# Kernel tuning notes

Measured on AMD Instinct MI355X. Metric: run time of the kernel, lower is better.

The kernel has to match this reference:

```python
import jax, jax.numpy as jnp
import numpy as np

B = 2          # point clouds per batch
N_PER = 80000  # occupied voxels per cloud
D = 64         # voxel grid resolution
K = 27         # 3x3x3 kernel volume
EPS = 1e-5


def _build_maps():
    rng = np.random.RandomState(0)
    coords = []
    for b in range(B):
        flat = rng.choice(D ** 3, N_PER, replace=False)
        x = flat // (D * D); y = (flat // D) % D; z = flat % D
        coords.append(np.stack([np.full(N_PER, b, np.int64), x, y, z], 1))
    coords = np.concatenate(coords, 0)  # [N,4] (batch, x, y, z)

    def make_grid(c, Dd):
        g = np.full(B * Dd ** 3, -1, np.int64)
        key = ((c[:, 0] * Dd + c[:, 1]) * Dd + c[:, 2]) * Dd + c[:, 3]
        g[key] = np.arange(len(c))
        return g

    offsets = np.array([[dx, dy, dz] for dx in (-1, 0, 1) for dy in (-1, 0, 1) for dz in (-1, 0, 1)], np.int64)

    def kernel_map(c, g, Dd):
        # per kernel offset: (input_row, output_row) pairs, padded to M with sentinel n
        n = len(c)
        ins, outs = [], []
        for off in offsets:
            sc = c[:, 1:] + off
            valid = np.all((sc >= 0) & (sc < Dd), 1)
            key = ((c[:, 0] * Dd + sc[:, 0]) * Dd + sc[:, 1]) * Dd + sc[:, 2]
            row = np.where(valid, g[np.clip(key, 0, len(g) - 1)], -1)
            m = row >= 0
            ins.append(row[m]); outs.append(np.nonzero(m)[0])
        M = max(len(a) for a in ins)
        ki = np.full((K, M), n, np.int32); ko = np.full((K, M), n, np.int32)
        for k in range(K):
            ki[k, :len(ins[k])] = ins[k]; ko[k, :len(outs[k])] = outs[k]
        return ki, ko

    km_in, km_out = kernel_map(coords, make_grid(coords, D), D)

    # maxpool k2/s2: each voxel maps to exactly one pooled coordinate floor(c/2)
    Dp = D // 2
    pc = coords.copy(); pc[:, 1:] //= 2
    pkey = ((pc[:, 0] * Dp + pc[:, 1]) * Dp + pc[:, 2]) * Dp + pc[:, 3]
    ukey, pool_seg = np.unique(pkey, return_inverse=True)
    pz = ukey % Dp; py = (ukey // Dp) % Dp; px = (ukey // (Dp * Dp)) % Dp; pb = ukey // (Dp ** 3)
    pcoords = np.stack([pb, px, py, pz], 1)
    km2_in, km2_out = kernel_map(pcoords, make_grid(pcoords, Dp), Dp)
    return len(coords), len(pcoords), km_in, km_out, pool_seg.astype(np.int32), km2_in, km2_out


N, N_POOL, _KM_IN, _KM_OUT, _POOL_SEG, _KM2_IN, _KM2_OUT = _build_maps()


def setup_inputs() -> dict:
    key = jax.random.key(0)
    ks = jax.random.split(key, 4)
    f32 = jnp.float32
    return {
        "feats": jax.random.normal(ks[0], (N, 1), f32),
        "W1": jax.random.normal(ks[1], (K, 1, 64), f32) * 0.2,
        "b1": jnp.zeros((64,), f32),
        "g1": jnp.ones((64,), f32), "be1": jnp.zeros((64,), f32),
        "W2": jax.random.normal(ks[2], (K, 64, 64), f32) * 0.05,
        "b2": jnp.zeros((64,), f32),
        "g2": jnp.ones((64,), f32), "be2": jnp.zeros((64,), f32),
        "W3": jax.random.normal(ks[3], (K, 64, 128), f32) * 0.05,
        "b3": jnp.zeros((128,), f32),
        "g3": jnp.ones((128,), f32), "be3": jnp.zeros((128,), f32),
        "km_in": jnp.asarray(_KM_IN), "km_out": jnp.asarray(_KM_OUT),
        "pool_seg": jnp.asarray(_POOL_SEG),
        "km2_in": jnp.asarray(_KM2_IN), "km2_out": jnp.asarray(_KM2_OUT),
    }


def _sparse_conv(x, ki, ko, W, b):
    # gather-GEMM-scatter per kernel offset; sentinel index n hits padded zero row / dummy out row
    n = x.shape[0]
    xp = jnp.concatenate([x, jnp.zeros((1, x.shape[1]), x.dtype)], 0)
    out = jnp.zeros((n + 1, W.shape[2]), x.dtype)
    for k in range(K):
        out = out.at[ko[k]].add(xp[ki[k]] @ W[k])
    return out[:n] + b


def _bn_relu(x, g, b):
    # training-mode BatchNorm over all active voxels (biased variance), then ReLU
    mu = jnp.mean(x, 0)
    var = jnp.mean((x - mu) ** 2, 0)
    return jax.nn.relu(g * (x - mu) * jax.lax.rsqrt(var + EPS) + b)


def reference(feats, W1, b1, g1, be1, W2, b2, g2, be2, W3, b3, g3, be3,
              km_in, km_out, pool_seg, km2_in, km2_out):
    x = _bn_relu(_sparse_conv(feats, km_in, km_out, W1, b1), g1, be1)
    x = _bn_relu(_sparse_conv(x, km_in, km_out, W2, b2), g2, be2)
    # maxpool k2/s2: segment-max onto pooled coordinates
    x = jnp.full((N_POOL, x.shape[1]), -jnp.inf, x.dtype).at[pool_seg].max(x)
    x = _bn_relu(_sparse_conv(x, km2_in, km2_out, W3, b3), g3, be3)
    return x  # [N_POOL, 128]
```

## Files before the change

### kernel.cpp

```cpp
#include <hip/hip_runtime.h>

#define EPS 1e-5f
#define KK 27

typedef __bf16 bf16x8 __attribute__((ext_vector_type(8)));
typedef float f32x4 __attribute__((ext_vector_type(4)));

__device__ __forceinline__ unsigned short f2bf(float f) {
    union { float f; unsigned u; } v; v.f = f;
    unsigned r = v.u + 0x7fffu + ((v.u >> 16) & 1u);
    return (unsigned short)(r >> 16);
}
__device__ __forceinline__ float bf2f(unsigned short h) {
    union { unsigned u; float f; } v; v.u = ((unsigned)h) << 16; return v.f;
}

__device__ __forceinline__ f32x4 mfma16(bf16x8 a, bf16x8 b, f32x4 c) {
    return __builtin_amdgcn_mfma_f32_16x16x32_bf16(a, b, c, 0, 0, 0);
}

__global__ void fill_i32(int* __restrict__ p, long tot, int val) {
    long i = (long)blockIdx.x * blockDim.x + threadIdx.x;
    if (i < tot) p[i] = val;
}

__global__ void invert_map_g(const int* __restrict__ km_in, const int* __restrict__ km_out,
                             int* __restrict__ idxG, int M, int nrows) {
    long i = (long)blockIdx.x * blockDim.x + threadIdx.x;
    if (i >= (long)KK * M) return;
    int k = (int)(i / M);
    int ki = km_in[i];
    if (ki < nrows) {
        int ko = km_out[i];
        idxG[(long)(ko >> 5) * 1024 + k * 32 + (ko & 31)] = ki;
    }
}

__global__ void wt_frag(const float* __restrict__ W, unsigned short* __restrict__ Wt,
                        int Cin, int Cout) {
    long i = (long)blockIdx.x * blockDim.x + threadIdx.x;
    long tot = (long)KK * Cin * Cout;
    if (i >= tot) return;
    int k  = (int)(i / (Cin * Cout));
    int r  = (int)(i % (Cin * Cout));
    int ci = r / Cout, co = r % Cout;
    int t = co >> 4, m16 = co & 15;
    int s = ci >> 5, quad = (ci >> 3) & 3, j = ci & 7;
    int lane = quad * 16 + m16;
    long off = ((((long)k * (Cout >> 4) + t) * 2 + s) * 64 + lane) * 8 + j;
    Wt[off] = f2bf(W[i]);
}

__global__ void w1t_bf16(const float* __restrict__ W1, unsigned short* __restrict__ W1t) {
    int i = blockIdx.x * blockDim.x + threadIdx.x;
    if (i >= 64 * 32) return;
    int c = i / 32, kk = i % 32;
    W1t[i] = (kk < KK) ? f2bf(W1[kk * 64 + c]) : (unsigned short)0;
}

__global__ void stats_part(const float* __restrict__ p, int nblk, int width,
                           float* __restrict__ out) {
    int c = threadIdx.x;
    int b0 = blockIdx.x * 64;
    int b1 = b0 + 64 < nblk ? b0 + 64 : nblk;
    float acc = 0.f;
    for (int b = b0; b < b1; ++b) acc += p[(long)b * width + c];
    atomicAdd(&out[c], acc);
}

__global__ __launch_bounds__(256, 2) void conv1_mfma(const float* __restrict__ feats,
                                                     const unsigned short* __restrict__ W1t,
                                                     const int* __restrict__ idxG, int n,
                                                     unsigned short* __restrict__ out,
                                                     float* __restrict__ partial) {
    __shared__ __align__(16) int lidx[4][1024];
    __shared__ float sstat[4][128];
    int tid = threadIdx.x;
    int wave = tid >> 6, lane = tid & 63;
    int m16 = lane & 15, quad = lane >> 4;
    long tile = (long)blockIdx.x * 4 + wave;
    long j0 = tile * 32;
    bool valid = (j0 < n);
    long jb = valid ? (j0 >> 5) : 0;

    {
        const int* src = idxG + jb * 1024;
        #pragma unroll
        for (int i = 0; i < 4; ++i)
            __builtin_amdgcn_global_load_lds(
                (const __attribute__((address_space(1))) unsigned*)(src + i * 256 + lane * 4),
                (__attribute__((address_space(3))) unsigned*)(&lidx[wave][i * 256]),
                16, 0, 0);
    }
    asm volatile("s_waitcnt vmcnt(0)" ::: "memory");
    const int* lip = &lidx[wave][0];

    int idx[2][8];
    #pragma unroll
    for (int i = 0; i < 8; ++i) {
        int kk = quad * 8 + i;
        bool kv = (kk < KK);
        idx[0][i] = (valid && kv) ? lip[kk * 32 + m16] : n;
        idx[1][i] = (valid && kv) ? lip[kk * 32 + 16 + m16] : n;
    }
    float f[2][8];
    #pragma unroll
    for (int i = 0; i < 8; ++i)
        #pragma unroll
        for (int t2 = 0; t2 < 2; ++t2) {
            int r = idx[t2][i];
            f[t2][i] = (r < n) ? feats[r] : 0.f;
        }

    union { bf16x8 v; unsigned short s[8]; } a[2];
    #pragma unroll
    for (int t2 = 0; t2 < 2; ++t2)
        #pragma unroll
        for (int i = 0; i < 8; ++i) a[t2].s[i] = f2bf(f[t2][i]);

    f32x4 acc[2][4];
    #pragma unroll
    for (int t2 = 0; t2 < 2; ++t2)
        #pragma unroll
        for (int t = 0; t < 4; ++t) acc[t2][t] = (f32x4){0.f, 0.f, 0.f, 0.f};

    const unsigned short* wb = W1t + quad * 8;
    #pragma unroll
    for (int t = 0; t < 4; ++t) {
        bf16x8 b = *(const bf16x8*)(wb + (t * 16 + m16) * 32);
        acc[0][t] = mfma16(a[0].v, b, acc[0][t]);
        acc[1][t] = mfma16(a[1].v, b, acc[1][t]);
    }

    asm volatile("" ::: "memory");
    unsigned short* sb = (unsigned short*)&lidx[wave][0];
    #pragma unroll
    for (int t2 = 0; t2 < 2; ++t2)
        #pragma unroll
        for (int t = 0; t < 4; ++t)
            #pragma unroll
            for (int r2 = 0; r2 < 4; ++r2)
                sb[(t2 * 16 + quad * 4 + r2) * 64 + t * 16 + m16] = f2bf(acc[t2][t][r2]);
    asm volatile("s_waitcnt lgkmcnt(0)" ::: "memory");
    #pragma unroll
    for (int i = 0; i < 4; ++i) {
        int row = i * 8 + (lane >> 3);
        long rr = j0 + row;
        if (rr < n)
            *(bf16x8*)(out + rr * 64 + (lane & 7) * 8) =
                *(const bf16x8*)(sb + row * 64 + (lane & 7) * 8);
    }

    #pragma unroll
    for (int t = 0; t < 4; ++t) {
        float s = 0.f, q = 0.f;
        #pragma unroll
        for (int t2 = 0; t2 < 2; ++t2)
            #pragma unroll
            for (int r2 = 0; r2 < 4; ++r2) { float v = acc[t2][t][r2]; s += v; q += v * v; }
        s += __shfl_xor(s, 16); q += __shfl_xor(q, 16);
        s += __shfl_xor(s, 32); q += __shfl_xor(q, 32);
        if (quad == 0) {
            sstat[wave][t * 16 + m16] = s;
            sstat[wave][64 + t * 16 + m16] = q;
        }
    }
    __syncthreads();
    if (tid < 128) {
        float p = sstat[0][tid] + sstat[1][tid] + sstat[2][tid] + sstat[3][tid];
        partial[(long)blockIdx.x * 128 + tid] = p;
    }
}

__global__ void bnrelu1_vec(unsigned short* __restrict__ x, const float* __restrict__ stats,
                            const float* __restrict__ g, const float* __restrict__ be, long n) {
    __shared__ float sc[64], sh[64];
    int tid = threadIdx.x;
    if (tid < 64) {
        float mu  = stats[tid] / (float)n;
        float var = stats[64 + tid] / (float)n - mu * mu;
        float s   = g[tid] * rsqrtf(var + EPS);
        sc[tid] = s; sh[tid] = be[tid] - mu * s;
    }
    __syncthreads();
    long i = (long)blockIdx.x * 256 + tid;
    long tot = (n + 1) * 8;
    if (i >= tot) return;
    long j = i >> 3; int c0 = (int)(i & 7) * 8;
    union { bf16x8 v; unsigned short s[8]; } u, o;
    if (j < n) {
        u.v = *(const bf16x8*)(x + j * 64 + c0);
        #pragma unroll
        for (int t = 0; t < 8; ++t) {
            float f = bf2f(u.s[t]) * sc[c0 + t] + sh[c0 + t];
            o.s[t] = f2bf(f > 0.f ? f : 0.f);
        }
    } else {
        #pragma unroll
        for (int t = 0; t < 8; ++t) o.s[t] = 0;
    }
    *(bf16x8*)(x + j * 64 + c0) = o.v;
}

template <int NT, bool BF16OUT>
__global__ __launch_bounds__(256, 2) void conv_pipe(const unsigned short* __restrict__ xin,
                                                    const unsigned short* __restrict__ Wt,
                                                    const int* __restrict__ idxG,
                                                    void* __restrict__ outv, int n,
                                                    float* __restrict__ partial) {
    constexpr int COUT = NT * 16;
    constexpr int SLICE = COUT * 64 * 2;
    constexpr int ROUNDS = SLICE / 4096;
    __shared__ __align__(16) int lidx[4][1024];
    __shared__ __align__(16) char bbuf[3][SLICE];
    __shared__ float sstat[4][2 * COUT];

    int tid = threadIdx.x;
    int wave = tid >> 6, lane = tid & 63;
    int m16 = lane & 15, quad = lane >> 4;
    long tile = (long)blockIdx.x * 4 + wave;
    long j0 = tile * 32;
    bool valid = (j0 < n);
    long jb = valid ? (j0 >> 5) : 0;

    auto stageB = [&](int k, int slot) {
        const char* src = (const char*)Wt + (long)k * SLICE;
        #pragma unroll
        for (int r = 0; r < ROUNDS; ++r)
            __builtin_amdgcn_global_load_lds(
                (const __attribute__((address_space(1))) unsigned*)(src + r * 4096 + wave * 1024 + lane * 16),
                (__attribute__((address_space(3))) unsigned*)(&bbuf[slot][r * 4096 + wave * 1024]),
                16, 0, 0);
    };

    {
        const int* src = idxG + jb * 1024;
        #pragma unroll
        for (int i = 0; i < 4; ++i)
            __builtin_amdgcn_global_load_lds(
                (const __attribute__((address_space(1))) unsigned*)(src + i * 256 + lane * 4),
                (__attribute__((address_space(3))) unsigned*)(&lidx[wave][i * 256]),
                16, 0, 0);
    }
    stageB(0, 0);
    if constexpr (ROUNDS == 2) asm volatile("s_waitcnt vmcnt(2)" ::: "memory");
    else                       asm volatile("s_waitcnt vmcnt(4)" ::: "memory");

    const int* lip = &lidx[wave][m16];
    bf16x8 ar[3][2][2];
    auto loadA = [&](int k, int slot) {
        int r0 = valid ? lip[k * 32] : n;
        int r1 = valid ? lip[k * 32 + 16] : n;
        const unsigned short* a0 = xin + (long)r0 * 64 + quad * 8;
        const unsigned short* a1 = xin + (long)r1 * 64 + quad * 8;
        ar[slot][0][0] = *(const bf16x8*)a0;
        ar[slot][0][1] = *(const bf16x8*)(a0 + 32);
        ar[slot][1][0] = *(const bf16x8*)a1;
        ar[slot][1][1] = *(const bf16x8*)(a1 + 32);
    };
    loadA(0, 0);
    stageB(1, 1);
    loadA(1, 1);

    f32x4 acc[2][NT];
    #pragma unroll
    for (int t2 = 0; t2 < 2; ++t2)
        #pragma unroll
        for (int t = 0; t < NT; ++t) acc[t2][t] = (f32x4){0.f, 0.f, 0.f, 0.f};

    #pragma unroll
    for (int k = 0; k < KK; ++k) {
        if (k < KK - 1) {
            if constexpr (ROUNDS == 2) asm volatile("s_waitcnt vmcnt(6)" ::: "memory");
            else                       asm volatile("s_waitcnt vmcnt(8)" ::: "memory");
        } else {
            asm volatile("s_waitcnt vmcnt(0)" ::: "memory");
        }
        __builtin_amdgcn_s_barrier();
        __builtin_amdgcn_sched_barrier(0);
        if (k + 2 < KK) {
            stageB(k + 2, (k + 2) % 3);
            loadA(k + 2, (k + 2) % 3);
        }
        const char* bs = &bbuf[k % 3][0];
        __builtin_amdgcn_s_setprio(1);
        #pragma unroll
        for (int s = 0; s < 2; ++s)
            #pragma unroll
            for (int t = 0; t < NT; ++t) {
                bf16x8 b = *(const bf16x8*)(bs + ((t * 2 + s) * 64 + lane) * 16);
                acc[0][t] = mfma16(ar[k % 3][0][s], b, acc[0][t]);
                acc[1][t] = mfma16(ar[k % 3][1][s], b, acc[1][t]);
            }
        __builtin_amdgcn_s_setprio(0);
    }

    asm volatile("" ::: "memory");
    if constexpr (BF16OUT) {
        unsigned short* sb = (unsigned short*)&lidx[wave][0];
        #pragma unroll
        for (int t2 = 0; t2 < 2; ++t2)
            #pragma unroll
            for (int t = 0; t < NT; ++t)
                #pragma unroll
                for (int r2 = 0; r2 < 4; ++r2)
                    sb[(t2 * 16 + quad * 4 + r2) * 64 + t * 16 + m16] = f2bf(acc[t2][t][r2]);
        asm volatile("s_waitcnt lgkmcnt(0)" ::: "memory");
        #pragma unroll
        for (int i = 0; i < 4; ++i) {
            int row = i * 8 + (lane >> 3);
            long rr = j0 + row;
            if (rr < n)
                *(bf16x8*)((unsigned short*)outv + rr * 64 + (lane & 7) * 8) =
                    *(const bf16x8*)(sb + row * 64 + (lane & 7) * 8);
        }
        asm volatile("" ::: "memory");
    } else if constexpr (COUT == 64) {
        float* sb = (float*)&lidx[wave][0];
        #pragma unroll
        for (int t2 = 0; t2 < 2; ++t2) {
            #pragma unroll
            for (int t = 0; t < NT; ++t)
                #pragma unroll
                for (int r2 = 0; r2 < 4; ++r2)
                    sb[(quad * 4 + r2) * COUT + t * 16 + m16] = acc[t2][t][r2];
            asm volatile("s_waitcnt lgkmcnt(0)" ::: "memory");
            #pragma unroll
            for (int i = 0; i < 4; ++i) {
                int row = i * 4 + (lane >> 4);
                long rr = j0 + t2 * 16 + row;
                if (rr < n)
                    *(float4*)((float*)outv + rr * COUT + (lane & 15) * 4) =
                        *(const float4*)(sb + row * COUT + (lane & 15) * 4);
            }
            asm volatile("" ::: "memory");
        }
    } else {
        float* sb = (float*)&lidx[wave][0];
        #pragma unroll
        for (int p = 0; p < 4; ++p) {
            const int t2p = p >> 1;
            const int qbase = (p & 1) * 2;
            if ((quad >> 1) == (p & 1)) {
                int lrb = (quad - qbase) * 4;
                #pragma unroll
                for (int t = 0; t < NT; ++t)
                    #pragma unroll
                    for (int r2 = 0; r2 < 4; ++r2)
                        sb[(lrb + r2) * 128 + t * 16 + m16] = acc[t2p][t][r2];
            }
            asm volatile("s_waitcnt lgkmcnt(0)" ::: "memory");
            #pragma unroll
            for (int i = 0; i < 4; ++i) {
                int f = i * 64 + lane;
                int row = f >> 5, c4 = f & 31;
                long rr = j0 + p * 8 + row;
                if (rr < n)
                    *(float4*)((float*)outv + rr * 128 + c4 * 4) =
                        *(const float4*)(sb + row * 128 + c4 * 4);
            }
            asm volatile("" ::: "memory");
        }
    }

    #pragma unroll
    for (int t = 0; t < NT; ++t) {
        float s = 0.f, q = 0.f;
        #pragma unroll
        for (int t2 = 0; t2 < 2; ++t2)
            #pragma unroll
            for (int r2 = 0; r2 < 4; ++r2) { float v = acc[t2][t][r2]; s += v; q += v * v; }
        s += __shfl_xor(s, 16); q += __shfl_xor(q, 16);
        s += __shfl_xor(s, 32); q += __shfl_xor(q, 32);
        if (quad == 0) {
            sstat[wave][t * 16 + m16] = s;
            sstat[wave][COUT + t * 16 + m16] = q;
        }
    }
    __syncthreads();
    if (tid < 2 * COUT) {
        float p = sstat[0][tid] + sstat[1][tid] + sstat[2][tid] + sstat[3][tid];
        partial[(long)blockIdx.x * (2 * COUT) + tid] = p;
    }
}

__global__ void pool_kernel(const unsigned short* __restrict__ x, const float* __restrict__ stats,
                            const float* __restrict__ g, const float* __restrict__ be,
                            const int* __restrict__ seg, long n, unsigned* __restrict__ pooled) {
    long j = (long)blockIdx.x * 4 + threadIdx.y;
    if (j >= n) return;
    int c = threadIdx.x;
    float mu  = stats[c] / (float)n;
    float var = stats[64 + c] / (float)n - mu * mu;
    float rs  = rsqrtf(var + EPS);
    float v   = g[c] * (bf2f(x[j * 64 + c]) - mu) * rs + be[c];
    if (v < 0.f) v = 0.f;
    atomicMax(&pooled[(long)seg[j] * 64 + c], __float_as_uint(v));
}

__global__ void pooled_bf16_vec(const unsigned* __restrict__ pooled, long np,
                                unsigned short* __restrict__ out) {
    long i = (long)blockIdx.x * 256 + threadIdx.x;
    long tot = (np + 1) * 8;
    if (i >= tot) return;
    long j = i >> 3; int c0 = (int)(i & 7) * 8;
    union { bf16x8 v; unsigned short s[8]; } o;
    if (j < np) {
        #pragma unroll
        for (int t = 0; t < 8; ++t)
            o.s[t] = f2bf(__uint_as_float(pooled[j * 64 + c0 + t]));
    } else {
        #pragma unroll
        for (int t = 0; t < 8; ++t) o.s[t] = 0;
    }
    *(bf16x8*)(out + j * 64 + c0) = o.v;
}

__global__ void bnrelu_out_vec(float* __restrict__ x, const float* __restrict__ stats,
                               const float* __restrict__ g, const float* __restrict__ be,
                               long n) {
    __shared__ float sc[128], sh[128];
    int tid = threadIdx.x;
    if (tid < 128) {
        float mu  = stats[tid] / (float)n;
        float var = stats[128 + tid] / (float)n - mu * mu;
        float s   = g[tid] * rsqrtf(var + EPS);
        sc[tid] = s; sh[tid] = be[tid] - mu * s;
    }
    __syncthreads();
    long i = (long)blockIdx.x * 256 + tid;
    long tot = n * 32;
    if (i >= tot) return;
    int c0 = (int)(i & 31) * 4;
    float4 v = ((float4*)x)[i];
    v.x = v.x * sc[c0]     + sh[c0];     v.x = v.x > 0.f ? v.x : 0.f;
    v.y = v.y * sc[c0 + 1] + sh[c0 + 1]; v.y = v.y > 0.f ? v.y : 0.f;
    v.z = v.z * sc[c0 + 2] + sh[c0 + 2]; v.z = v.z > 0.f ? v.z : 0.f;
    v.w = v.w * sc[c0 + 3] + sh[c0 + 3]; v.w = v.w > 0.f ? v.w : 0.f;
    ((float4*)x)[i] = v;
}

extern "C" void kernel_launch(void* const* d_in, const int* in_sizes, int n_in,
                              void* d_out, int out_size, void* d_ws, size_t ws_size,
                              hipStream_t stream) {
    const float* feats = (const float*)d_in[0];
    const float* W1  = (const float*)d_in[1];
    const float* g1  = (const float*)d_in[3];
    const float* be1 = (const float*)d_in[4];
    const float* W2  = (const float*)d_in[5];
    const float* g2  = (const float*)d_in[7];
    const float* be2 = (const float*)d_in[8];
    const float* W3  = (const float*)d_in[9];
    const float* g3  = (const float*)d_in[11];
    const float* be3 = (const float*)d_in[12];
    const int* km_in   = (const int*)d_in[13];
    const int* km_out  = (const int*)d_in[14];
    const int* pool_seg = (const int*)d_in[15];
    const int* km2_in  = (const int*)d_in[16];
    const int* km2_out = (const int*)d_in[17];

    const int n  = in_sizes[0];
    const int M  = in_sizes[13] / KK;
    const int np = out_size / 128;
    const int M2 = in_sizes[16] / KK;
    const long nb1 = n / 32 + 2;
    const long nb2 = np / 32 + 2;

    const int waves1 = (n + 31) / 32;
    const int nblk1  = (waves1 + 3) / 4;
    const int waves2 = (n + 31) / 32;
    const int nblk2  = (waves2 + 3) / 4;
    const int waves3 = (np + 31) / 32;
    const int nblk3  = (waves3 + 3) / 4;


    char* ws = (char*)d_ws;
    size_t off = 0;
    auto alloc = [&](size_t bytes) -> char* {
        char* p = ws + off;
        off += (bytes + 255) & ~(size_t)255;
        return p;
    };
    int* idxG1 = (int*)alloc(nb1 * 4096);
    int* idxG2 = (int*)alloc(nb2 * 4096);
    unsigned short* W1t = (unsigned short*)alloc(64 * 32 * 2);
    unsigned short* W2t = (unsigned short*)alloc((size_t)KK * 64 * 64 * 2);
    unsigned short* W3t = (unsigned short*)alloc((size_t)KK * 128 * 64 * 2);
    float* stats = (float*)alloc(4096);
    unsigned short* x1n = (unsigned short*)alloc((size_t)(n + 1) * 64 * 2);
    unsigned short* x2r = (unsigned short*)alloc((size_t)n * 64 * 2);
    unsigned* pooled = (unsigned*)alloc((size_t)np * 64 * 4);
    unsigned short* xpn = (unsigned short*)alloc((size_t)(np + 1) * 64 * 2);
    float* part1 = (float*)alloc((size_t)nblk1 * 128 * 4);
    float* part2 = (float*)alloc((size_t)nblk2 * 128 * 4);
    float* part3 = (float*)alloc((size_t)nblk3 * 256 * 4);
    float* x3 = (float*)d_out;
    if (off > ws_size) return;

    float* stats1 = stats;
    float* stats2 = stats + 128;
    float* stats3 = stats + 256;

    hipMemsetAsync(stats, 0, 4096, stream);
    hipMemsetAsync(pooled, 0, (size_t)np * 64 * 4, stream);

    {
        long t1 = nb1 * 1024;
        fill_i32<<<(int)((t1 + 255) / 256), 256, 0, stream>>>(idxG1, t1, n);
        long t2 = nb2 * 1024;
        fill_i32<<<(int)((t2 + 255) / 256), 256, 0, stream>>>(idxG2, t2, np);
        long e1 = (long)KK * M;
        invert_map_g<<<(int)((e1 + 255) / 256), 256, 0, stream>>>(km_in, km_out, idxG1, M, n);
        long e2 = (long)KK * M2;
        invert_map_g<<<(int)((e2 + 255) / 256), 256, 0, stream>>>(km2_in, km2_out, idxG2, M2, np);
    }
    {
        w1t_bf16<<<8, 256, 0, stream>>>(W1, W1t);
        long t2 = (long)KK * 64 * 64;
        wt_frag<<<(int)((t2 + 255) / 256), 256, 0, stream>>>(W2, W2t, 64, 64);
        long t3 = (long)KK * 64 * 128;
        wt_frag<<<(int)((t3 + 255) / 256), 256, 0, stream>>>(W3, W3t, 64, 128);
    }

    conv1_mfma<<<nblk1, 256, 0, stream>>>(feats, W1t, idxG1, n, x1n, part1);
    stats_part<<<(nblk1 + 63) / 64, 128, 0, stream>>>(part1, nblk1, 128, stats1);
    {
        long tot = ((long)(n + 1) * 8 + 255) / 256;
        bnrelu1_vec<<<(int)tot, 256, 0, stream>>>(x1n, stats1, g1, be1, n);
    }
    conv_pipe<4, true><<<nblk2, 256, 0, stream>>>(x1n, W2t, idxG1, x2r, n, part2);
    stats_part<<<(nblk2 + 63) / 64, 128, 0, stream>>>(part2, nblk2, 128, stats2);
    pool_kernel<<<(n + 3) / 4, dim3(64, 4), 0, stream>>>(x2r, stats2, g2, be2, pool_seg, n, pooled);
    {
        long tot = ((long)(np + 1) * 8 + 255) / 256;
        pooled_bf16_vec<<<(int)tot, 256, 0, stream>>>(pooled, np, xpn);
    }
    conv_pipe<8, false><<<nblk3, 256, 0, stream>>>(xpn, W3t, idxG2, x3, np, part3);
    stats_part<<<(nblk3 + 63) / 64, 256, 0, stream>>>(part3, nblk3, 256, stats3);
    {
        long tot = ((long)np * 32 + 255) / 256;
        bnrelu_out_vec<<<(int)tot, 256, 0, stream>>>(x3, stats3, g3, be3, np);
    }
}
```

Baseline: 375.0 us.

## Reorder voxels by pooling segment and replace atomic max-pool with segmented reduction

Computes a counting-sort permutation of the input voxels grouped by their pooled cell (histogram, prefix scan, scatter). It then permutes the features and kernel maps so conv1 and conv2 work in sorted order. Max-pooling then becomes a contiguous segmented max with no atomics and no separate float-to-bf16 pass. Workgroup IDs in conv_pipe are also swizzled. This costs several extra small preprocessing kernels, and scatter_perm's atomics make the order inside each segment nondeterministic, which does not affect the max.

New measurement: 413.2 us. +10.2%, slower.

```diff
diff --git a/kernel.cpp b/kernel.cpp
--- a/kernel.cpp
+++ b/kernel.cpp
@@ -19,9 +19,85 @@
     return __builtin_amdgcn_mfma_f32_16x16x32_bf16(a, b, c, 0, 0, 0);
 }
 
+__device__ __forceinline__ long swz_bid(long bid, long nwg) {
+    long q = nwg >> 3, r = nwg & 7;
+    long x = bid & 7, o = bid >> 3;
+    long base = (x < r) ? x * (q + 1) : r * (q + 1) + (x - r) * q;
+    return base + o;
+}
+
+__global__ void hist_seg(const int* __restrict__ seg, long n, int* __restrict__ cnt) {
+    long i = (long)blockIdx.x * 256 + threadIdx.x;
+    if (i < n) atomicAdd(&cnt[seg[i]], 1);
+}
+
+__global__ void scan_block256(const int* __restrict__ cnt, int np,
+                              int* __restrict__ excl, int* __restrict__ bsum) {
+    __shared__ int s[256];
+    int i = blockIdx.x * 256 + threadIdx.x;
+    int v = (i < np) ? cnt[i] : 0;
+    s[threadIdx.x] = v; __syncthreads();
+    #pragma unroll
+    for (int d = 1; d < 256; d <<= 1) {
+        int t = (threadIdx.x >= d) ? s[threadIdx.x - d] : 0;
+        __syncthreads();
+        s[threadIdx.x] += t;
+        __syncthreads();
+    }
+    if (i < np) excl[i] = s[threadIdx.x] - v;
+    if (threadIdx.x == 255) bsum[blockIdx.x] = s[255];
+}
+
+__global__ void scan_tops256(int* __restrict__ bsum, int nb) {
+    __shared__ int s[256];
+    int v = (threadIdx.x < nb) ? bsum[threadIdx.x] : 0;
+    s[threadIdx.x] = v; __syncthreads();
+    #pragma unroll
+    for (int d = 1; d < 256; d <<= 1) {
+        int t = (threadIdx.x >= d) ? s[threadIdx.x - d] : 0;
+        __syncthreads();
+        s[threadIdx.x] += t;
+        __syncthreads();
+    }
+    if (threadIdx.x < nb) bsum[threadIdx.x] = s[threadIdx.x] - v;
+}
+
+__global__ void scan_add(int* __restrict__ excl, const int* __restrict__ bsum, int np) {
+    int i = blockIdx.x * 256 + threadIdx.x;
+    if (i < np) excl[i] += bsum[blockIdx.x];
+}
+
+__global__ void scatter_perm(const int* __restrict__ seg, long n, int* __restrict__ ofs,
+                             int* __restrict__ perm, int* __restrict__ inv) {
+    long i = (long)blockIdx.x * 256 + threadIdx.x;
+    if (i >= n) return;
+    int p = atomicAdd(&ofs[seg[i]], 1);
+    perm[p] = (int)i;
+    inv[i] = p;
+}
+
+__global__ void permute_f32(const float* __restrict__ src, const int* __restrict__ perm,
+                            float* __restrict__ dst, long n) {
+    long i = (long)blockIdx.x * 256 + threadIdx.x;
+    if (i < n) dst[i] = src[perm[i]];
+}
+
 __global__ void fill_i32(int* __restrict__ p, long tot, int val) {
     long i = (long)blockIdx.x * blockDim.x + threadIdx.x;
     if (i < tot) p[i] = val;
+}
+
+__global__ void invert_map_p(const int* __restrict__ km_in, const int* __restrict__ km_out,
+                             const int* __restrict__ inv, int* __restrict__ idxG,
+                             int M, int nrows) {
+    long i = (long)blockIdx.x * blockDim.x + threadIdx.x;
+    if (i >= (long)KK * M) return;
+    int k = (int)(i / M);
+    int ki = km_in[i];
+    if (ki < nrows) {
+        int po = inv[km_out[i]];
+        idxG[(long)(po >> 5) * 1024 + k * 32 + (po & 31)] = inv[ki];
+    }
 }
 
 __global__ void invert_map_g(const int* __restrict__ km_in, const int* __restrict__ km_out,
@@ -218,7 +294,7 @@
     int tid = threadIdx.x;
     int wave = tid >> 6, lane = tid & 63;
     int m16 = lane & 15, quad = lane >> 4;
-    long tile = (long)blockIdx.x * 4 + wave;
+    long tile = swz_bid(blockIdx.x, gridDim.x) * 4 + wave;
     long j0 = tile * 32;
     bool valid = (j0 < n);
     long jb = valid ? (j0 >> 5) : 0;
@@ -384,36 +460,27 @@
     }
 }
 
-__global__ void pool_kernel(const unsigned short* __restrict__ x, const float* __restrict__ stats,
+__global__ void pool_sorted(const unsigned short* __restrict__ x, const float* __restrict__ stats,
                             const float* __restrict__ g, const float* __restrict__ be,
-                            const int* __restrict__ seg, long n, unsigned* __restrict__ pooled) {
-    long j = (long)blockIdx.x * 4 + threadIdx.y;
-    if (j >= n) return;
-    int c = threadIdx.x;
+                            const int* __restrict__ ofs, const int* __restrict__ cnt,
+                            long n, int np, unsigned short* __restrict__ xpn) {
+    int wave = threadIdx.x >> 6, c = threadIdx.x & 63;
+    long p = (long)blockIdx.x * 4 + wave;
+    if (p > np) return;
+    if (p == np) { xpn[p * 64 + c] = 0; return; }
     float mu  = stats[c] / (float)n;
     float var = stats[64 + c] / (float)n - mu * mu;
-    float rs  = rsqrtf(var + EPS);
-    float v   = g[c] * (bf2f(x[j * 64 + c]) - mu) * rs + be[c];
-    if (v < 0.f) v = 0.f;
-    atomicMax(&pooled[(long)seg[j] * 64 + c], __float_as_uint(v));
-}
-
-__global__ void pooled_bf16_vec(const unsigned* __restrict__ pooled, long np,
-                                unsigned short* __restrict__ out) {
-    long i = (long)blockIdx.x * 256 + threadIdx.x;
-    long tot = (np + 1) * 8;
-    if (i >= tot) return;
-    long j = i >> 3; int c0 = (int)(i & 7) * 8;
-    union { bf16x8 v; unsigned short s[8]; } o;
-    if (j < np) {
-        #pragma unroll
-        for (int t = 0; t < 8; ++t)
-            o.s[t] = f2bf(__uint_as_float(pooled[j * 64 + c0 + t]));
-    } else {
-        #pragma unroll
-        for (int t = 0; t < 8; ++t) o.s[t] = 0;
-    }
-    *(bf16x8*)(out + j * 64 + c0) = o.v;
+    float sc  = g[c] * rsqrtf(var + EPS);
+    float sh  = be[c] - mu * sc;
+    int e = ofs[p];
+    int s = e - cnt[p];
+    float m = 0.f;
+    for (int r = s; r < e; ++r) {
+        float v = bf2f(x[(long)r * 64 + c]) * sc + sh;
+        if (v < 0.f) v = 0.f;
+        if (v > m) m = v;
+    }
+    xpn[p * 64 + c] = f2bf(m);
 }
 
 __global__ void bnrelu_out_vec(float* __restrict__ x, const float* __restrict__ stats,
@@ -489,11 +556,16 @@
     float* stats = (float*)alloc(4096);
     unsigned short* x1n = (unsigned short*)alloc((size_t)(n + 1) * 64 * 2);
     unsigned short* x2r = (unsigned short*)alloc((size_t)n * 64 * 2);
-    unsigned* pooled = (unsigned*)alloc((size_t)np * 64 * 4);
     unsigned short* xpn = (unsigned short*)alloc((size_t)(np + 1) * 64 * 2);
     float* part1 = (float*)alloc((size_t)nblk1 * 128 * 4);
     float* part2 = (float*)alloc((size_t)nblk2 * 128 * 4);
     float* part3 = (float*)alloc((size_t)nblk3 * 256 * 4);
+    int* cnt  = (int*)alloc((size_t)np * 4);
+    int* ofs  = (int*)alloc((size_t)np * 4);
+    int* bsum = (int*)alloc(256 * 4);
+    int* perm = (int*)alloc((size_t)n * 4);
+    int* invp = (int*)alloc((size_t)n * 4);
+    float* featp = (float*)alloc((size_t)n * 4);
     float* x3 = (float*)d_out;
     if (off > ws_size) return;
 
@@ -502,7 +574,18 @@
     float* stats3 = stats + 256;
 
     hipMemsetAsync(stats, 0, 4096, stream);
-    hipMemsetAsync(pooled, 0, (size_t)np * 64 * 4, stream);
+    hipMemsetAsync(cnt, 0, (size_t)np * 4, stream);
+
+    {
+        int nblk = (int)((n + 255) / 256);
+        hist_seg<<<nblk, 256, 0, stream>>>(pool_seg, n, cnt);
+        int nb = (np + 255) / 256;
+        scan_block256<<<nb, 256, 0, stream>>>(cnt, np, ofs, bsum);
+        scan_tops256<<<1, 256, 0, stream>>>(bsum, nb);
+        scan_add<<<nb, 256, 0, stream>>>(ofs, bsum, np);
+        scatter_perm<<<nblk, 256, 0, stream>>>(pool_seg, n, ofs, perm, invp);
+        permute_f32<<<nblk, 256, 0, stream>>>(feats, perm, featp, n);
+    }
 
     {
         long t1 = nb1 * 1024;
@@ -510,7 +593,7 @@
         long t2 = nb2 * 1024;
         fill_i32<<<(int)((t2 + 255) / 256), 256, 0, stream>>>(idxG2, t2, np);
         long e1 = (long)KK * M;
-        invert_map_g<<<(int)((e1 + 255) / 256), 256, 0, stream>>>(km_in, km_out, idxG1, M, n);
+        invert_map_p<<<(int)((e1 + 255) / 256), 256, 0, stream>>>(km_in, km_out, invp, idxG1, M, n);
         long e2 = (long)KK * M2;
         invert_map_g<<<(int)((e2 + 255) / 256), 256, 0, stream>>>(km2_in, km2_out, idxG2, M2, np);
     }
@@ -522,7 +605,7 @@
         wt_frag<<<(int)((t3 + 255) / 256), 256, 0, stream>>>(W3, W3t, 64, 128);
     }
 
-    conv1_mfma<<<nblk1, 256, 0, stream>>>(feats, W1t, idxG1, n, x1n, part1);
+    conv1_mfma<<<nblk1, 256, 0, stream>>>(featp, W1t, idxG1, n, x1n, part1);
     stats_part<<<(nblk1 + 63) / 64, 128, 0, stream>>>(part1, nblk1, 128, stats1);
     {
         long tot = ((long)(n + 1) * 8 + 255) / 256;
@@ -530,10 +613,9 @@
     }
     conv_pipe<4, true><<<nblk2, 256, 0, stream>>>(x1n, W2t, idxG1, x2r, n, part2);
     stats_part<<<(nblk2 + 63) / 64, 128, 0, stream>>>(part2, nblk2, 128, stats2);
-    pool_kernel<<<(n + 3) / 4, dim3(64, 4), 0, stream>>>(x2r, stats2, g2, be2, pool_seg, n, pooled);
-    {
-        long tot = ((long)(np + 1) * 8 + 255) / 256;
-        pooled_bf16_vec<<<(int)tot, 256, 0, stream>>>(pooled, np, xpn);
+    {
+        int pblk = (np + 1 + 3) / 4;
+        pool_sorted<<<pblk, 256, 0, stream>>>(x2r, stats2, g2, be2, ofs, cnt, n, np, xpn);
     }
     conv_pipe<8, false><<<nblk3, 256, 0, stream>>>(xpn, W3t, idxG2, x3, np, part3);
     stats_part<<<(nblk3 + 63) / 64, 256, 0, stream>>>(part3, nblk3, 256, stats3);
```
